# Kernel optimization log

Measured on AMD Instinct MI355X. Metric: run time of the kernel, lower is better.

Reference implementation:

```python
import jax, jax.numpy as jnp
import numpy as np

NUM_HEADS = 16
HEAD_DIM = 64  # d_model // num_heads = 1024 // 16
NUM_BUCKETS = 20


def setup_inputs() -> dict:
    key = jax.random.key(0)
    ks = jax.random.split(key, 5)
    B, S, D = 2, 2048, 1024
    v = jax.random.normal(ks[0], (B, S, D), dtype=jnp.float32)
    k = jax.random.normal(ks[1], (B, S, D), dtype=jnp.float32)
    q = jax.random.normal(ks[2], (B, S, D), dtype=jnp.float32)
    mask = jax.random.randint(ks[3], (B, S, S), 0, 2).astype(jnp.bool_)
    diff_matrix = jax.random.randint(ks[4], (B, S, S), 0, NUM_BUCKETS)
    rel_bias = jax.random.normal(jax.random.fold_in(key, 7), (NUM_BUCKETS, NUM_HEADS), dtype=jnp.float32)
    return {"v": v, "k": k, "q": q, "mask": mask, "diff_matrix": diff_matrix, "rel_bias": rel_bias}


def _split_heads(x):
    B, S, _ = x.shape
    return x.reshape(B, S, NUM_HEADS, HEAD_DIM).transpose(0, 2, 1, 3)  # [B,H,S,hd]


def reference(v, k, q, mask, diff_matrix, rel_bias):
    B, S, D = q.shape
    qh, kh, vh = _split_heads(q), _split_heads(k), _split_heads(v)
    scale = 1.0 / jnp.sqrt(jnp.float32(HEAD_DIM))
    scores = jnp.einsum('bhqd,bhkd->bhqk', qh, kh) * scale  # [B,H,S,S]
    # relative bias: gather [B,S,S,H] -> [B,H,S,S]
    bias = rel_bias[diff_matrix].transpose(0, 3, 1, 2)
    att = jax.nn.silu(scores + bias)
    att = jnp.where(mask[:, None, :, :], att, 0.0)
    av = jnp.einsum('bhqk,bhkd->bhqd', att, vh)  # [B,H,S,hd]
    return av.transpose(0, 2, 1, 3).reshape(B, S, D)
```

## Files before the change

### kernel.cpp

```cpp
#include <hip/hip_runtime.h>
#include <hip/hip_fp16.h>
#include <cstdint>
#include <cstddef>

#define SEQ 2048
#define DM 1024
#define NH 16
#define NB 20

typedef _Float16 half8 __attribute__((ext_vector_type(8)));
typedef _Float16 half4 __attribute__((ext_vector_type(4)));
typedef _Float16 h2v __attribute__((ext_vector_type(2)));
typedef float f32x4 __attribute__((ext_vector_type(4)));
typedef float f32x2 __attribute__((ext_vector_type(2)));
typedef int i32x4 __attribute__((ext_vector_type(4)));
typedef unsigned int u32;
typedef unsigned int u32x2 __attribute__((ext_vector_type(2)));

#define KF_HALVES 4194304
#define VF_HALVES 4194304

__global__ __launch_bounds__(256) void pa_prep(
    const float* __restrict__ v, const float* __restrict__ k,
    const int* __restrict__ diff, const int* __restrict__ mask,
    _Float16* __restrict__ KF, _Float16* __restrict__ VF,
    unsigned char* __restrict__ PB) {
  const int bid = blockIdx.x, tid = threadIdx.x;
  if (bid < 2048) {
    int img = bid >> 4;
    int bb = img >> 6, kt = img & 63;
    int tix = ((bid & 15) << 8) | tid;
    int r = tix >> 7;
    int c0 = (tix & 127) << 3;
    const float* src = k + ((size_t)(bb * SEQ + kt * 32 + r)) * DM + c0;
    f32x4 a = *(const f32x4*)src;
    f32x4 c = *(const f32x4*)(src + 4);
    half8 o = {(_Float16)a[0], (_Float16)a[1], (_Float16)a[2], (_Float16)a[3],
               (_Float16)c[0], (_Float16)c[1], (_Float16)c[2], (_Float16)c[3]};
    int h = c0 >> 6, dh = (c0 >> 5) & 1, g4 = (c0 >> 3) & 3;
    int k2 = r >> 4, l16 = r & 15;
    int lane = g4 * 16 + l16;
    size_t off = ((size_t)((bb * 16 + h) * 64 + kt)) * 2048 + (k2 * 2 + dh) * 512 + lane * 8;
    *(half8*)(KF + off) = o;
  } else if (bid < 3072) {
    int b3 = bid - 2048;
    int img = b3 >> 3;
    int bb = img >> 6, kt = img & 63;
    int tix = ((b3 & 7) << 8) | tid;
    int kq = tix >> 8;
    int k2 = kq >> 2, g4 = kq & 3;
    int d0 = (tix & 255) << 2;
    const float* src = v + ((size_t)(bb * SEQ + kt * 32 + k2 * 16 + g4 * 4)) * DM + d0;
    f32x4 m0 = *(const f32x4*)(src);
    f32x4 m1 = *(const f32x4*)(src + DM);
    f32x4 m2 = *(const f32x4*)(src + 2 * DM);
    f32x4 m3 = *(const f32x4*)(src + 3 * DM);
#pragma unroll
    for (int i = 0; i < 4; ++i) {
      int d = d0 + i;
      int l16 = d & 15, dt = (d >> 4) & 3, h = d >> 6;
      int lane = g4 * 16 + l16;
      half4 o = {(_Float16)m0[i], (_Float16)m1[i], (_Float16)m2[i], (_Float16)m3[i]};
      size_t off = ((size_t)((bb * 16 + h) * 64 + kt)) * 2048 + dt * 512 + lane * 8 + k2 * 4;
      *(half4*)(VF + off) = o;
    }
  } else {
    int b4 = bid - 3072;
    int job = b4 >> 5;
    int bb = job >> 6, qblk = job & 63;
    int tix = ((b4 & 31) << 8) | tid;
    int kt = tix >> 7;
    int rem = tix & 127;
    int g4 = rem & 3, l16 = (rem >> 2) & 15, qs = rem >> 6;
    int lane = g4 * 16 + l16;
    int qrow = qblk * 32 + qs * 16 + l16;
    size_t rowbase = ((size_t)(bb * SEQ + qrow)) * SEQ;
    u32x2 wds;
#pragma unroll
    for (int k2 = 0; k2 < 2; ++k2) {
      int kk = kt * 32 + k2 * 16 + g4 * 4;
      i32x4 dv = *(const i32x4*)(diff + rowbase + kk);
      i32x4 mv = *(const i32x4*)(mask + rowbase + kk);
      u32 bk[4];
#pragma unroll
      for (int r = 0; r < 4; ++r) bk[r] = mv[r] ? (u32)dv[r] : 20u;
      u32 pi01 = bk[0] * 21 + bk[1];
      u32 pi23 = bk[2] * 21 + bk[3];
      wds[k2] = pi01 | (pi23 << 16);
    }
    size_t off = ((size_t)job) * 65536 + (size_t)kt * 1024 + (size_t)lane * 16 + (size_t)qs * 8;
    *(u32x2*)(PB + off) = wds;
  }
}

__device__ __forceinline__ void gll16(const _Float16* g, _Float16* l) {
  __builtin_amdgcn_global_load_lds(
      (const __attribute__((address_space(1))) unsigned int*)g,
      (__attribute__((address_space(3))) unsigned int*)l, 16, 0, 0);
}

__device__ __forceinline__ half4 silu4nb(const f32x4& s) {
  h2v x01 = __builtin_bit_cast(h2v, __builtin_amdgcn_cvt_pkrtz(s[0], s[1]));
  h2v x23 = __builtin_bit_cast(h2v, __builtin_amdgcn_cvt_pkrtz(s[2], s[3]));
  const h2v NL2E = {(_Float16)-1.44269504f, (_Float16)-1.44269504f};
  const h2v ONE = {(_Float16)1.0f, (_Float16)1.0f};
  h2v m01 = x01 * NL2E, m23 = x23 * NL2E;
  h2v e01 = __builtin_bit_cast(h2v, h2exp2(__builtin_bit_cast(__half2, m01)));
  h2v e23 = __builtin_bit_cast(h2v, h2exp2(__builtin_bit_cast(__half2, m23)));
  h2v d01 = e01 + ONE, d23 = e23 + ONE;
  h2v y01 = x01 * __builtin_bit_cast(h2v, h2rcp(__builtin_bit_cast(__half2, d01)));
  h2v y23 = x23 * __builtin_bit_cast(h2v, h2rcp(__builtin_bit_cast(__half2, d23)));
  return (half4){y01[0], y01[1], y23[0], y23[1]};
}

struct BiasSet { f32x4 b[2][2]; };

__global__ __launch_bounds__(512, 4) void pa_main(
    const _Float16* __restrict__ KF, const _Float16* __restrict__ VF,
    const unsigned char* __restrict__ PB, const float* __restrict__ q,
    const float* __restrict__ relbias, float* __restrict__ out) {
  __shared__ __align__(16) _Float16 ringK[4][2048];
  __shared__ f32x2 tabF[441];

  const int tid = threadIdx.x, lane = tid & 63, wid = tid >> 6;
  const int w4 = wid & 3, par = wid >> 2;
  const int l16 = lane & 15, g4 = lane >> 4;
  const int xcd = blockIdx.x & 7;
  const int i = blockIdx.x >> 3;
  const int b = xcd >> 2;
  const int hg = xcd & 3;
  const int h = hg * 4 + (i & 3);
  const int qgrp = i >> 2;
  const int qblk = qgrp * 4 + w4;
  const int qbase = qblk * 32;

  for (int e = tid; e < 441; e += 512) {
    int bi = e / 21, bj = e - bi * 21;
    float vi = (bi < NB) ? relbias[bi * NH + h] : -30000.0f;
    float vj = (bj < NB) ? relbias[bj * NH + h] : -30000.0f;
    tabF[e] = (f32x2){vi, vj};
  }

  half8 qf[2][2];
#pragma unroll
  for (int qs = 0; qs < 2; ++qs)
#pragma unroll
    for (int dh = 0; dh < 2; ++dh) {
      const float* s = q + ((size_t)(b * SEQ + qbase + qs * 16 + l16)) * DM + h * 64 + dh * 32 + g4 * 8;
      f32x4 a = *(const f32x4*)s;
      f32x4 c = *(const f32x4*)(s + 4);
      qf[qs][dh] = {(_Float16)(a[0] * 0.125f), (_Float16)(a[1] * 0.125f),
                    (_Float16)(a[2] * 0.125f), (_Float16)(a[3] * 0.125f),
                    (_Float16)(c[0] * 0.125f), (_Float16)(c[1] * 0.125f),
                    (_Float16)(c[2] * 0.125f), (_Float16)(c[3] * 0.125f)};
    }

  f32x4 acc[2][4];
#pragma unroll
  for (int qs = 0; qs < 2; ++qs)
#pragma unroll
    for (int dt = 0; dt < 4; ++dt) acc[qs][dt] = (f32x4){0.f, 0.f, 0.f, 0.f};

  const _Float16* kfb = KF + ((size_t)((b * 16 + h) * 64)) * 2048 + lane * 8;
  const _Float16* vfb = VF + ((size_t)((b * 16 + h) * 64)) * 2048 + lane * 8;
  const unsigned char* pbb = PB + ((size_t)(b * 64 + qblk)) * 65536 + lane * 16;
  const int c512 = w4 * 512;

#define STAGE(T) gll16(kfb + (size_t)(T) * 2048 + c512, &ringK[(T) & 3][c512])
#define CLMP(T) ((T) < 64 ? (T) : 63)

#define GATHER(BS, PQ)                                                 \
  do {                                                                 \
    _Pragma("unroll") for (int qs = 0; qs < 2; ++qs)                   \
      _Pragma("unroll") for (int k2 = 0; k2 < 2; ++k2) {               \
        u32 w = (u32)PQ[qs * 2 + k2];                                  \
        f32x2 p01 = tabF[w & 0xffffu];                                 \
        f32x2 p23 = tabF[w >> 16];                                     \
        BS.b[qs][k2] = (f32x4){p01[0], p01[1], p23[0], p23[1]};        \
      }                                                                \
  } while (0)

#define COMPUTE(T, BS)                                                                       \
  do {                                                                                       \
    int sl_ = (T) & 3;                                                                       \
    half8 vvr[4];                                                                            \
    _Pragma("unroll") for (int j = 0; j < 4; ++j)                                            \
      vvr[j] = *(const half8*)(vfb + (size_t)(T) * 2048 + j * 512);           \
    half8 kfr[4];                                                                            \
    _Pragma("unroll") for (int j = 0; j < 4; ++j)                                            \
      kfr[j] = *(const half8*)&ringK[sl_][j * 512 + lane * 8];                 \
    f32x4 sa[2][2];                                                                          \
    _Pragma("unroll") for (int qs = 0; qs < 2; ++qs)                                         \
      _Pragma("unroll") for (int k2 = 0; k2 < 2; ++k2) {                                     \
        sa[qs][k2] = __builtin_amdgcn_mfma_f32_16x16x32_f16(kfr[k2 * 2 + 0], qf[qs][0],      \
                                                            BS.b[qs][k2], 0, 0, 0);          \
        sa[qs][k2] = __builtin_amdgcn_mfma_f32_16x16x32_f16(kfr[k2 * 2 + 1], qf[qs][1],      \
                                                            sa[qs][k2], 0, 0, 0);            \
      }                                                                                      \
    half8 pf8[2];                                                                            \
    _Pragma("unroll") for (int qs = 0; qs < 2; ++qs) {                                       \
      half4 p0 = silu4nb(sa[qs][0]);                                                         \
      half4 p1 = silu4nb(sa[qs][1]);                                                         \
      pf8[qs] = (half8){p0[0], p0[1], p0[2], p0[3], p1[0], p1[1], p1[2], p1[3]};             \
    }                                                                                        \
    _Pragma("unroll") for (int qs = 0; qs < 2; ++qs)                                         \
      _Pragma("unroll") for (int dt = 0; dt < 4; ++dt)                                       \
        acc[qs][dt] = __builtin_amdgcn_mfma_f32_16x16x32_f16(pf8[qs], vvr[dt],               \
                                                             acc[qs][dt], 0, 0, 0);          \
  } while (0)

  BiasSet bias;
  i32x4 pqCur, pqNext;

  STAGE(par);
  STAGE(par + 2);
  pqCur = *(const i32x4*)(pbb + (size_t)par * 1024);
  __syncthreads();

  for (int p = 0; p < 32; ++p) {
    const int T = 2 * p + par;
    pqNext = *(const i32x4*)(pbb + (size_t)CLMP(T + 2) * 1024);
    __builtin_amdgcn_sched_barrier(0);
    GATHER(bias, pqCur);
    COMPUTE(T, bias);
    __syncthreads();
    if (T + 4 < 64) STAGE(T + 4);
    pqCur = pqNext;
    __syncthreads();
  }
#undef STAGE
#undef CLMP
#undef GATHER
#undef COMPUTE

  f32x4* red = (f32x4*)ringK;
#pragma unroll
  for (int qs = 0; qs < 2; ++qs) {
    __syncthreads();
    if (par == 1) {
#pragma unroll
      for (int dt = 0; dt < 4; ++dt) red[(w4 * 64 + lane) * 4 + dt] = acc[qs][dt];
    }
    __syncthreads();
    if (par == 0) {
#pragma unroll
      for (int dt = 0; dt < 4; ++dt) {
        f32x4 sum = acc[qs][dt] + red[(w4 * 64 + lane) * 4 + dt];
#pragma unroll
        for (int r = 0; r < 4; ++r) {
          int qrow = qbase + qs * 16 + g4 * 4 + r;
          int d = h * 64 + dt * 16 + l16;
          out[((size_t)(b * SEQ) + qrow) * DM + d] = sum[r];
        }
      }
    }
  }
}

extern "C" void kernel_launch(void* const* d_in, const int* in_sizes, int n_in,
                              void* d_out, int out_size, void* d_ws, size_t ws_size,
                              hipStream_t stream) {
  const float* v = (const float*)d_in[0];
  const float* k = (const float*)d_in[1];
  const float* q = (const float*)d_in[2];
  const int* mask = (const int*)d_in[3];
  const int* diff = (const int*)d_in[4];
  const float* relbias = (const float*)d_in[5];
  float* out = (float*)d_out;

  _Float16* KF = (_Float16*)d_ws;
  _Float16* VF = KF + KF_HALVES;
  unsigned char* PB = (unsigned char*)(VF + VF_HALVES);
  if (ws_size < (size_t)25165824) return;

  pa_prep<<<7168, 256, 0, stream>>>(v, k, diff, mask, KF, VF, PB);
  pa_main<<<512, 512, 0, stream>>>(KF, VF, PB, q, relbias, out);
}
```

Measured before the change: 87.30 us.

## Split key tiles four ways across waves and double block count

Each block now covers two 32-row query blocks instead of four. The four wave groups split the key tiles four ways (stride 4), where before two parity groups split them two ways. The K ring buffer grows to 8 slots and the launch count doubles to 1024 blocks. Staging now happens before compute, so each iteration needs only one barrier. The final reduction sums partial accumulators from four waves through LDS. The aim is more parallelism and less sync overhead, at the cost of a bigger reduction and a higher occupancy target in the launch bounds, which may cause register spills.

```diff
diff --git a/kernel.cpp b/kernel.cpp
--- a/kernel.cpp
+++ b/kernel.cpp
@@ -115,23 +115,23 @@
 
 struct BiasSet { f32x4 b[2][2]; };
 
-__global__ __launch_bounds__(512, 4) void pa_main(
+__global__ __launch_bounds__(512, 8) void pa_main(
     const _Float16* __restrict__ KF, const _Float16* __restrict__ VF,
     const unsigned char* __restrict__ PB, const float* __restrict__ q,
     const float* __restrict__ relbias, float* __restrict__ out) {
-  __shared__ __align__(16) _Float16 ringK[4][2048];
+  __shared__ __align__(16) _Float16 ringK[8][2048];
   __shared__ f32x2 tabF[441];
 
   const int tid = threadIdx.x, lane = tid & 63, wid = tid >> 6;
-  const int w4 = wid & 3, par = wid >> 2;
+  const int qt = wid & 3, w2 = wid >> 2;
   const int l16 = lane & 15, g4 = lane >> 4;
   const int xcd = blockIdx.x & 7;
   const int i = blockIdx.x >> 3;
   const int b = xcd >> 2;
   const int hg = xcd & 3;
   const int h = hg * 4 + (i & 3);
-  const int qgrp = i >> 2;
-  const int qblk = qgrp * 4 + w4;
+  const int qgrp2 = i >> 2;
+  const int qblk = qgrp2 * 2 + w2;
   const int qbase = qblk * 32;
 
   for (int e = tid; e < 441; e += 512) {
@@ -164,9 +164,13 @@
   const _Float16* kfb = KF + ((size_t)((b * 16 + h) * 64)) * 2048 + lane * 8;
   const _Float16* vfb = VF + ((size_t)((b * 16 + h) * 64)) * 2048 + lane * 8;
   const unsigned char* pbb = PB + ((size_t)(b * 64 + qblk)) * 65536 + lane * 16;
-  const int c512 = w4 * 512;
-
-#define STAGE(T) gll16(kfb + (size_t)(T) * 2048 + c512, &ringK[(T) & 3][c512])
+  const int ch = w2 * 1024;
+
+#define STAGE(T)                                                            \
+  do {                                                                      \
+    gll16(kfb + (size_t)(T) * 2048 + ch, &ringK[(T) & 7][ch]);              \
+    gll16(kfb + (size_t)(T) * 2048 + ch + 512, &ringK[(T) & 7][ch + 512]);  \
+  } while (0)
 #define CLMP(T) ((T) < 64 ? (T) : 63)
 
 #define GATHER(BS, PQ)                                                 \
@@ -182,7 +186,7 @@
 
 #define COMPUTE(T, BS)                                                                       \
   do {                                                                                       \
-    int sl_ = (T) & 3;                                                                       \
+    int sl_ = (T) & 7;                                                                       \
     half8 vvr[4];                                                                            \
     _Pragma("unroll") for (int j = 0; j < 4; ++j)                                            \
       vvr[j] = *(const half8*)(vfb + (size_t)(T) * 2048 + j * 512);           \
@@ -212,21 +216,19 @@
   BiasSet bias;
   i32x4 pqCur, pqNext;
 
-  STAGE(par);
-  STAGE(par + 2);
-  pqCur = *(const i32x4*)(pbb + (size_t)par * 1024);
+  STAGE(qt);
+  pqCur = *(const i32x4*)(pbb + (size_t)qt * 1024);
   __syncthreads();
 
-  for (int p = 0; p < 32; ++p) {
-    const int T = 2 * p + par;
-    pqNext = *(const i32x4*)(pbb + (size_t)CLMP(T + 2) * 1024);
+  for (int p = 0; p < 16; ++p) {
+    const int T = 4 * p + qt;
+    if (T + 4 < 64) STAGE(T + 4);
+    pqNext = *(const i32x4*)(pbb + (size_t)CLMP(T + 4) * 1024);
     __builtin_amdgcn_sched_barrier(0);
     GATHER(bias, pqCur);
     COMPUTE(T, bias);
     __syncthreads();
-    if (T + 4 < 64) STAGE(T + 4);
     pqCur = pqNext;
-    __syncthreads();
   }
 #undef STAGE
 #undef CLMP
@@ -237,15 +239,19 @@
 #pragma unroll
   for (int qs = 0; qs < 2; ++qs) {
     __syncthreads();
-    if (par == 1) {
-#pragma unroll
-      for (int dt = 0; dt < 4; ++dt) red[(w4 * 64 + lane) * 4 + dt] = acc[qs][dt];
+    if (qt > 0) {
+#pragma unroll
+      for (int dt = 0; dt < 4; ++dt)
+        red[((qt - 1) * 2 + w2) * 256 + lane * 4 + dt] = acc[qs][dt];
     }
     __syncthreads();
-    if (par == 0) {
+    if (qt == 0) {
 #pragma unroll
       for (int dt = 0; dt < 4; ++dt) {
-        f32x4 sum = acc[qs][dt] + red[(w4 * 64 + lane) * 4 + dt];
+        f32x4 sum = acc[qs][dt];
+#pragma unroll
+        for (int qq = 1; qq < 4; ++qq)
+          sum += red[((qq - 1) * 2 + w2) * 256 + lane * 4 + dt];
 #pragma unroll
         for (int r = 0; r < 4; ++r) {
           int qrow = qbase + qs * 16 + g4 * 4 + r;
@@ -274,5 +280,5 @@
   if (ws_size < (size_t)25165824) return;
 
   pa_prep<<<7168, 256, 0, stream>>>(v, k, diff, mask, KF, VF, PB);
-  pa_main<<<512, 512, 0, stream>>>(KF, VF, PB, q, relbias, out);
-}
+  pa_main<<<1024, 512, 0, stream>>>(KF, VF, PB, q, relbias, out);
+}
```

Result: slower. 295.0 us (+237.9%).
